# Optimization experiments

Hardware: AMD Instinct MI355X
Metric: run time of the kernel (lower is better)

## Reference

```python
import jax, jax.numpy as jnp
import numpy as np

B, T, H, WD = 512, 168, 512, 4  # batch, seq_len, hidden_dim, WEATHER_DIM


def setup_inputs() -> dict:
    key = jax.random.key(0)
    ks = jax.random.split(key, 11)
    sc = 1.0 / np.sqrt(H)

    def u(k, shape):
        return jax.random.uniform(k, shape, jnp.float32, -sc, sc)

    return {
        "inputs": jax.random.normal(ks[0], (B, T, WD + 1), dtype=jnp.float32),
        # layer 1: input_sz=1 (counts)
        "W1": u(ks[1], (1, 4 * H)),
        "U1": u(ks[2], (H, 4 * H)),
        "V1": u(ks[3], (WD, 4 * H)),
        "b1": u(ks[4], (4 * H,)),
        # layer 2: input_sz=H
        "W2": u(ks[5], (H, 4 * H)),
        "U2": u(ks[6], (H, 4 * H)),
        "V2": u(ks[7], (WD, 4 * H)),
        "b2": u(ks[8], (4 * H,)),
        # final linear head (xavier-ish init)
        "fc_w": u(ks[9], (1, H)),
        "fc_b": jnp.zeros((1,), jnp.float32),
    }


def pew_lstm(x, w, W, U, V, b):
    """Weather-conditioned LSTM layer.
    x: [B,T,I] main input, w: [B,T,WD] weather.
    Gates = x@W + h@U + weather@V + b (weather injected each step).
    Returns hidden sequence [B,T,H]."""
    bs = x.shape[0]
    hdim = U.shape[0]
    # precompute all non-recurrent contributions once: [B,T,4H]
    pre = jnp.einsum('bti,ig->btg', x, W) + jnp.einsum('btw,wg->btg', w, V) + b

    def step(carry, pre_t):
        h, c = carry
        gates = pre_t + h @ U              # [B,4H]
        i, f, g, o = jnp.split(gates, 4, axis=-1)
        c = jax.nn.sigmoid(f) * c + jax.nn.sigmoid(i) * jnp.tanh(g)
        h = jax.nn.sigmoid(o) * jnp.tanh(c)
        return (h, c), h

    h0 = jnp.zeros((bs, hdim), x.dtype)
    (_, _), hs = jax.lax.scan(step, (h0, h0), pre.transpose(1, 0, 2))
    return hs.transpose(1, 0, 2)  # [B,T,H]


def reference(inputs, W1, U1, V1, b1, W2, U2, V2, b2, fc_w, fc_b):
    weather = inputs[:, :, :-1]   # [B,T,WD]
    counts = inputs[:, :, -1:]    # [B,T,1]
    h1 = pew_lstm(counts, weather, W1, U1, V1, b1)
    h2 = pew_lstm(h1, weather, W2, U2, V2, b2)
    out = h2.reshape(-1, h2.shape[-1]) @ fc_w.T + fc_b  # [B*T,1]
    return out.reshape(-1)
```

## Files before the change

kernel.cpp:

```cpp
#include <hip/hip_runtime.h>
#include <cstdint>
#include <cstddef>

typedef unsigned int   u32;
typedef unsigned short u16;
typedef unsigned long long u64;
typedef __attribute__((ext_vector_type(8))) short bf16x8;
typedef __attribute__((ext_vector_type(4))) float f32x4;

#define B_  512
#define T_  168
#define H_  512

#define OFF_U1P   (0u)
#define OFF_UW2P  (2u*1024*1024)
#define OFF_H1    (6u*1024*1024)
#define OFF_H2    (14u*1024*1024)
#define OFF_FLAGS (16u*1024*1024)
#define H_SLOT    262144u
#define NRING     8
#define FSTRIDE   64
#define SMEM_V6   (131072 + 6144 + 3072)

__device__ __forceinline__ u16 f2bf(float v){
  u32 u = __float_as_uint(v);
  return (u16)((u + 0x7fffu + ((u >> 16) & 1u)) >> 16);
}
__device__ __forceinline__ float bf2f(u16 b){ return __uint_as_float(((u32)b) << 16); }
__device__ __forceinline__ float sigm(float x){ return 1.f/(1.f + __expf(-x)); }
__device__ __forceinline__ float tanh_f(float x){
  float e = __expf(-2.f*fabsf(x));
  float t = (1.f - e)/(1.f + e);
  return (x < 0.f) ? -t : t;
}
__device__ __forceinline__ float sigm_f(float x){ return __fdividef(1.f, 1.f + __expf(-x)); }
__device__ __forceinline__ float tanh_ff(float x){
  float e = __expf(-2.f*fabsf(x));
  float t = __fdividef(1.f - e, 1.f + e);
  return (x < 0.f) ? -t : t;
}
__device__ __forceinline__ void spin_ge(int* p, int target){
  while (__hip_atomic_load(p, __ATOMIC_RELAXED, __HIP_MEMORY_SCOPE_AGENT) < target)
    __builtin_amdgcn_s_sleep(1);
}
__device__ __forceinline__ void async_cp16(const void* g, void* l){
  __builtin_amdgcn_global_load_lds((const __attribute__((address_space(1))) u32*)g,
                                   (__attribute__((address_space(3))) u32*)l, 16, 0, 0);
}
__device__ __forceinline__ bf16x8 plain_ld16(const u16* p){
  return *(const bf16x8*)p;
}
__device__ __forceinline__ bf16x8 ring_ld16(const u16* p){
  union { u64 q[2]; bf16x8 v; } u;
  u.q[0] = __hip_atomic_load((const u64*)p,     __ATOMIC_RELAXED, __HIP_MEMORY_SCOPE_AGENT);
  u.q[1] = __hip_atomic_load(((const u64*)p)+1, __ATOMIC_RELAXED, __HIP_MEMORY_SCOPE_AGENT);
  return u.v;
}
__device__ __forceinline__ void ring_st16(u16* p, uint4 v){
  u64 lo = ((u64)v.y << 32) | v.x;
  u64 hi = ((u64)v.w << 32) | v.z;
  __hip_atomic_store((u64*)p,     lo, __ATOMIC_RELAXED, __HIP_MEMORY_SCOPE_AGENT);
  __hip_atomic_store(((u64*)p)+1, hi, __ATOMIC_RELAXED, __HIP_MEMORY_SCOPE_AGENT);
}

__global__ void pack_w_kernel(const float* __restrict__ U1, const float* __restrict__ W2,
                              const float* __restrict__ U2, u16* __restrict__ U1p,
                              u16* __restrict__ UW2p)
{
  int idx = blockIdx.x*256 + threadIdx.x;
  int ln = idx & 63;
  int q8 = ((ln >> 4) << 3);
  int cl = ln & 15;
  if (idx < 16*128*64) {
    int kc = idx >> 13, ng = (idx >> 6) & 127;
    int row0 = kc*32 + q8, col = ng*16 + cl;
    u16* d = U1p + (size_t)idx*8;
    #pragma unroll
    for (int j=0;j<8;j++) d[j] = f2bf(U1[(size_t)(row0+j)*2048 + col]);
  } else {
    int i2 = idx - 16*128*64;
    if (i2 >= 32*128*64) return;
    int kc = i2 >> 13, ng = (i2 >> 6) & 127;
    int row0 = kc*32 + q8, col = ng*16 + cl;
    u16* d = UW2p + (size_t)i2*8;
    #pragma unroll
    for (int j=0;j<8;j++){
      int r = row0 + j;
      float v = (r < 512) ? W2[(size_t)r*2048 + col] : U2[(size_t)(r-512)*2048 + col];
      d[j] = f2bf(v);
    }
  }
}

__global__ void init_kernel(float* __restrict__ out, const float* __restrict__ fcb,
                            int* __restrict__ flags)
{
  int i = blockIdx.x*256 + threadIdx.x;
  if (i < 2048) flags[i] = 0;
  if (i < B_*T_) out[i] = fcb[0];
}


__device__ void run_l1_v6(char* smem, int blk, const float* __restrict__ inp,
                          const float* __restrict__ W1, const float* __restrict__ V,
                          const float* __restrict__ bias, char* __restrict__ ws)
{
  u16*  Bl   = (u16*)smem;
  u16*  hlds = (u16*)(smem + 131072);
  float* wlds = (float*)(smem + 131072 + 6144);
  constexpr int RS = 40;
  const int tid = threadIdx.x, w = tid>>6, ln = tid&63, col = ln&15, quad = ln>>4;
  const int bi = blk & 7, hj = blk >> 3, h0 = hj*32, bg = bi*4 + w;

  const u16* Upak = (const u16*)(ws + OFF_U1P);
  const u16* H1r  = (const u16*)(ws + OFF_H1);
  u16* Hw = (u16*)(ws + OFF_H1);
  int* done1 = (int*)(ws + OFF_FLAGS) + bi*FSTRIDE;
  int* done2 = (int*)(ws + OFF_FLAGS) + 1024 + (bi>>1)*FSTRIDE;

  #pragma unroll
  for (int p=0;p<32;p++){
    int pid = w*32 + p, kc = pid>>3, ngl = pid&7;
    int ng = (ngl>>1)*32 + hj*2 + (ngl&1);
    async_cp16(Upak + ((size_t)(kc*128+ng)*64 + ln)*8, Bl + (size_t)pid*512);
  }
  for (int idx=tid; idx<4*32*6; idx+=256){
    int gate = idx/192, rem = idx%192, hcol = rem/6, k = rem%6;
    int gcol = gate*512 + h0 + hcol;
    wlds[idx] = (k==0)? bias[gcol] : (k<=4 ? V[(size_t)(k-1)*2048 + gcol] : W1[gcol]);
  }

  float c[8];
  #pragma unroll
  for (int i=0;i<8;i++) c[i] = 0.f;
  const f32x4 vzero = {0.f,0.f,0.f,0.f};

  for (int t=0; t<T_; t++){
    if (tid==0){
      if (t>0)      spin_ge(done1, 16*t);
      if (t>=NRING) spin_ge(done2, 32*(t-NRING+1));
      __builtin_amdgcn_fence(__ATOMIC_ACQUIRE, "agent");
    }
    __syncthreads();

    f32x4 acc[8];
    #pragma unroll
    for (int i=0;i<8;i++) acc[i] = vzero;

    if (t > 0){
      const u16* ab = H1r + (size_t)((t-1)&7)*H_SLOT + (size_t)bg*16*512 + (size_t)ln*8;
      bf16x8 aw[8];
      #pragma unroll
      for (int i=0;i<8;i++) aw[i] = plain_ld16(ab + (size_t)i*512);
      #pragma unroll
      for (int kc=0; kc<16; kc++){
        bf16x8 av = aw[kc&7];
        if (kc < 8) aw[kc&7] = plain_ld16(ab + (size_t)(kc+8)*512);
        const u16* bb = Bl + (size_t)kc*8*512 + (size_t)ln*8;
        #pragma unroll
        for (int ngl=0; ngl<8; ngl++)
          acc[ngl] = __builtin_amdgcn_mfma_f32_16x16x32_bf16(
              av, *(const bf16x8*)(bb + (size_t)ngl*512), acc[ngl], 0,0,0);
      }
    }

    float inv[4][5];
    #pragma unroll
    for (int r=0;r<4;r++){
      const float* ip = inp + ((size_t)(bi*64 + w*16 + quad*4 + r)*T_ + t)*5;
      #pragma unroll
      for (int k=0;k<5;k++) inv[r][k] = ip[k];
    }
    #pragma unroll
    for (int hg=0; hg<2; hg++){
      float wv[4][6];
      #pragma unroll
      for (int gate=0; gate<4; gate++){
        const float* wp = wlds + (size_t)(gate*32 + hg*16 + col)*6;
        #pragma unroll
        for (int k=0;k<6;k++) wv[gate][k] = wp[k];
      }
      #pragma unroll
      for (int r=0;r<4;r++){
        float gv[4];
        #pragma unroll
        for (int gate=0; gate<4; gate++){
          gv[gate] = acc[gate*2+hg][r] + wv[gate][0]
                   + inv[r][0]*wv[gate][1] + inv[r][1]*wv[gate][2]
                   + inv[r][2]*wv[gate][3] + inv[r][3]*wv[gate][4]
                   + inv[r][4]*wv[gate][5];
        }
        float ig=sigm_f(gv[0]), fg=sigm_f(gv[1]), gg=tanh_ff(gv[2]), og=sigm_f(gv[3]);
        float cn = fg*c[hg*4+r] + ig*gg;
        c[hg*4+r] = cn;
        hlds[(size_t)(w*16 + quad*4 + r)*RS + hg*16 + col] = f2bf(og*tanh_ff(cn));
      }
    }
    {
      uint4 v = *(const uint4*)&hlds[(size_t)(w*16 + (ln&15))*RS + (ln>>4)*8];
      ring_st16(Hw + (size_t)(t&7)*H_SLOT + ((size_t)(bg*16 + hj)*64 + ln)*8, v);
    }
    __syncthreads();
    if (tid==0){
      __builtin_amdgcn_fence(__ATOMIC_RELEASE, "workgroup");
      __hip_atomic_fetch_add(done1, 1, __ATOMIC_RELAXED, __HIP_MEMORY_SCOPE_AGENT);
    }
  }
}

template<int KCEND>
__device__ __forceinline__ void l2_kloop(f32x4* accA, f32x4* accB, const u16* Bl,
                                         const u16* A1, const u16* A2,
                                         int bgA, int bgB, int ln)
{
  bf16x8 awA[8], awB[8];
  #pragma unroll
  for (int i=0;i<8;i++){
    awA[i] = plain_ld16(A1 + ((size_t)bgA*16 + i)*512 + (size_t)ln*8);
    awB[i] = plain_ld16(A1 + ((size_t)bgB*16 + i)*512 + (size_t)ln*8);
  }
  #pragma unroll
  for (int kc=0; kc<KCEND; kc++){
    bf16x8 avA = awA[kc&7], avB = awB[kc&7];
    if (kc+8 < KCEND){
      int k2 = kc+8;
      const u16* base = (k2 < 16) ? A1 : A2;
      int kcl = (k2 < 16) ? k2 : (k2-16);
      awA[kc&7] = plain_ld16(base + ((size_t)bgA*16 + kcl)*512 + (size_t)ln*8);
      awB[kc&7] = plain_ld16(base + ((size_t)bgB*16 + kcl)*512 + (size_t)ln*8);
    }
    const u16* bb = Bl + (size_t)kc*4*512 + (size_t)ln*8;
    #pragma unroll
    for (int ngl=0; ngl<4; ngl++){
      bf16x8 bf = *(const bf16x8*)(bb + (size_t)ngl*512);
      accA[ngl] = __builtin_amdgcn_mfma_f32_16x16x32_bf16(avA, bf, accA[ngl], 0,0,0);
      accB[ngl] = __builtin_amdgcn_mfma_f32_16x16x32_bf16(avB, bf, accB[ngl], 0,0,0);
    }
  }
}

__device__ void run_l2_v6(char* smem, int blk2, const float* __restrict__ inp,
                          const float* __restrict__ V, const float* __restrict__ bias,
                          const float* __restrict__ fcw, char* __restrict__ ws,
                          float* __restrict__ out)
{
  u16*  Bl   = (u16*)smem;
  u16*  hlds = (u16*)(smem + 131072);
  float* wlds = (float*)(smem + 131072 + 6144);
  constexpr int RS = 24;
  const int tid = threadIdx.x, w = tid>>6, ln = tid&63, col = ln&15, quad = ln>>4;
  const int bi2 = blk2 & 3, hj = blk2 >> 2, h0 = hj*16;
  const int bgA = bi2*8 + w, bgB = bgA + 4;

  const u16* Upak = (const u16*)(ws + OFF_UW2P);
  const u16* H1r  = (const u16*)(ws + OFF_H1);
  const u16* H2r  = (const u16*)(ws + OFF_H2);
  u16* Hw = (u16*)(ws + OFF_H2);
  int* flags = (int*)(ws + OFF_FLAGS);
  int* d1a = flags + (2*bi2)*FSTRIDE;
  int* d1b = flags + (2*bi2+1)*FSTRIDE;
  int* done2 = flags + 1024 + bi2*FSTRIDE;

  #pragma unroll
  for (int p=0;p<32;p++){
    int pid = w*32 + p, kc = pid>>2, ngl = pid&3;
    int ng = ngl*32 + hj;
    async_cp16(Upak + ((size_t)(kc*128+ng)*64 + ln)*8, Bl + (size_t)pid*512);
  }
  for (int idx=tid; idx<4*16*6; idx+=256){
    int gate = idx/96, rem = idx%96, hcol = rem/6, k = rem%6;
    int gcol = gate*512 + h0 + hcol;
    wlds[idx] = (k==0)? bias[gcol] : (k<=4 ? V[(size_t)(k-1)*2048 + gcol] : 0.f);
  }
  const float fcwr = fcw[h0 + col];

  float c[8];
  #pragma unroll
  for (int i=0;i<8;i++) c[i] = 0.f;
  const f32x4 vzero = {0.f,0.f,0.f,0.f};

  for (int t=0; t<T_; t++){
    if (tid==0){
      spin_ge(d1a, 16*(t+1));
      spin_ge(d1b, 16*(t+1));
      if (t>0) spin_ge(done2, 32*t);
      __builtin_amdgcn_fence(__ATOMIC_ACQUIRE, "agent");
    }
    __syncthreads();

    f32x4 accA[4], accB[4];
    #pragma unroll
    for (int i=0;i<4;i++){ accA[i] = vzero; accB[i] = vzero; }

    const u16* A1 = H1r + (size_t)(t&7)*H_SLOT;
    if (t > 0){
      const u16* A2 = H2r + (size_t)((t-1)&1)*H_SLOT;
      l2_kloop<32>(accA, accB, Bl, A1, A2, bgA, bgB, ln);
    } else {
      l2_kloop<16>(accA, accB, Bl, A1, A1, bgA, bgB, ln);
    }

    float wv[4][5];
    #pragma unroll
    for (int gate=0; gate<4; gate++){
      const float* wp = wlds + (size_t)(gate*16 + col)*6;
      #pragma unroll
      for (int k=0;k<5;k++) wv[gate][k] = wp[k];
    }
    float fcp[2][4];
    #pragma unroll
    for (int sel=0; sel<2; sel++){
      const f32x4* ac = sel ? accB : accA;
      #pragma unroll
      for (int r=0;r<4;r++){
        const float* ip = inp + ((size_t)(bi2*128 + sel*64 + w*16 + quad*4 + r)*T_ + t)*5;
        float i0=ip[0], i1=ip[1], i2=ip[2], i3=ip[3];
        float gv[4];
        #pragma unroll
        for (int gate=0; gate<4; gate++){
          gv[gate] = ac[gate][r] + wv[gate][0]
                   + i0*wv[gate][1] + i1*wv[gate][2] + i2*wv[gate][3] + i3*wv[gate][4];
        }
        float ig=sigm_f(gv[0]), fg=sigm_f(gv[1]), gg=tanh_ff(gv[2]), og=sigm_f(gv[3]);
        float cn = fg*c[sel*4+r] + ig*gg;
        c[sel*4+r] = cn;
        float h = og*tanh_ff(cn);
        fcp[sel][r] = h*fcwr;
        hlds[(size_t)(sel*64 + w*16 + quad*4 + r)*RS + col] = f2bf(h);
      }
    }
    #pragma unroll
    for (int sel=0; sel<2; sel++){
      #pragma unroll
      for (int r=0;r<4;r++){
        float v = fcp[sel][r];
        #pragma unroll
        for (int m=1;m<16;m<<=1) v += __shfl_xor(v, m, 16);
        if (col == 0)
          atomicAdd(&out[(size_t)(bi2*128 + sel*64 + w*16 + quad*4 + r)*T_ + t], v);
      }
    }
    {
      int sel = ln>>5, ch = (ln>>4)&1, m = ln&15;
      uint4 v = *(const uint4*)&hlds[(size_t)(sel*64 + w*16 + m)*RS + ch*8];
      int lp = ((hj&1)*2 + ch)*16 + m;
      int bgx = bi2*8 + sel*4 + w;
      ring_st16(Hw + (size_t)(t&1)*H_SLOT + ((size_t)(bgx*16 + (hj>>1))*64 + lp)*8, v);
    }
    __syncthreads();
    if (tid==0){
      __builtin_amdgcn_fence(__ATOMIC_RELEASE, "workgroup");
      __hip_atomic_fetch_add(done2, 1, __ATOMIC_RELAXED, __HIP_MEMORY_SCOPE_AGENT);
    }
  }
}

__global__ void __launch_bounds__(256, 1)
lstm_main_v6(const float* __restrict__ inp, const float* __restrict__ W1,
             const float* __restrict__ V1, const float* __restrict__ b1,
             const float* __restrict__ V2, const float* __restrict__ b2,
             const float* __restrict__ fcw, char* __restrict__ ws, float* __restrict__ out)
{
  extern __shared__ char smem[];
  int blk = blockIdx.x;
  if (blk < 128) run_l1_v6(smem, blk, inp, W1, V1, b1, ws);
  else           run_l2_v6(smem, blk-128, inp, V2, b2, fcw, ws, out);
}

template<int LAYER>
__device__ __forceinline__ void stage_B(u16* buf, const u16* __restrict__ Upak,
                                        int hj, int g, int w, int ln)
{
  constexpr int NGW = (LAYER==1)?16:8;
  constexpr int GKC = (LAYER==1)?2:4;
  #pragma unroll
  for (int p=0;p<8;p++){
    int pid = w*8 + p;
    int kci = pid / NGW;
    int ngl = pid % NGW;
    int gate = ngl / (NGW/4);
    int sub  = ngl % (NGW/4);
    int ng   = gate*32 + hj*(NGW/4) + sub;
    int kc   = g*GKC + kci;
    const u16* src = Upak + ((size_t)(kc*128 + ng)*64 + ln)*8;
    u16* dst = buf + (size_t)(kci*NGW + ngl)*512;
    async_cp16(src, dst);
  }
}

template<int LAYER>
__device__ __forceinline__ void preload_A(bf16x8* areg, const u16* __restrict__ A1,
                                          const u16* __restrict__ A2, int bg, int g, int ln)
{
  constexpr int GKC = (LAYER==1)?2:4;
  #pragma unroll
  for (int kci=0;kci<GKC;kci++){
    int kc = g*GKC + kci;
    const u16* base = A1; int kcl = kc;
    if (LAYER==2 && kc >= 16){ base = A2; kcl = kc - 16; }
    areg[kci] = ring_ld16(base + ((size_t)bg*16 + kcl)*512 + (size_t)ln*8);
  }
}

template<int LAYER>
__device__ void run_layer(u16 (*Bbuf)[16384], int blk,
                          const float* __restrict__ inp,
                          const float* __restrict__ W1,
                          const float* __restrict__ V,
                          const float* __restrict__ bias,
                          const float* __restrict__ fcw,
                          char* __restrict__ ws,
                          float* __restrict__ out)
{
  constexpr int HT  = (LAYER==1)?64:32;
  constexpr int HGN = (LAYER==1)?4:2;
  constexpr int NGW = (LAYER==1)?16:8;
  constexpr int GKC = (LAYER==1)?2:4;
  constexpr int RS  = (LAYER==1)?72:40;
  constexpr int KCP = (LAYER==1)?2:1;
  constexpr int NPIECE = 4*KCP;

  const int tid = threadIdx.x;
  const int w    = tid >> 6;
  const int ln   = tid & 63;
  const int col  = ln & 15;
  const int quad = ln >> 4;
  const int bi = (LAYER==1) ? (blk >> 3) : ((blk-64) >> 4);
  const int hj = (LAYER==1) ? (blk & 7)  : ((blk-64) & 15);
  const int h0 = hj * HT;
  const int bg = bi*4 + w;

  const u16* Upak = (const u16*)(ws + ((LAYER==1)?OFF_U1P:OFF_UW2P));
  const u16* H1r  = (const u16*)(ws + OFF_H1);
  const u16* H2r  = (const u16*)(ws + OFF_H2);
  u16* Hw  = (u16*)(ws + ((LAYER==1)?OFF_H1:OFF_H2));
  int* done1 = (int*)(ws + OFF_FLAGS);
  int* done2 = (int*)(ws + OFF_FLAGS) + 1024;
  u16* hlds  = &Bbuf[0][0];

  float fcwr[HGN];
  if (LAYER==2){
    #pragma unroll
    for (int hg=0; hg<HGN; hg++) fcwr[hg] = fcw[h0 + hg*16 + col];
  }
  float c[HGN*4];
  #pragma unroll
  for (int i=0;i<HGN*4;i++) c[i] = 0.f;
  const f32x4 vzero = {0.f,0.f,0.f,0.f};

  if (LAYER==2) stage_B<LAYER>(Bbuf[0], Upak, hj, 0, w, ln);

  for (int t=0; t<T_; t++){
    if (tid == 0){
      if (LAYER==1){
        if (t > 0)      spin_ge(&done1[bi*FSTRIDE], 8*t);
        if (t >= NRING) spin_ge(&done2[bi*FSTRIDE], 16*(t-NRING+1));
      } else {
        spin_ge(&done1[bi*FSTRIDE], 8*(t+1));
        if (t > 0) spin_ge(&done2[bi*FSTRIDE], 16*t);
      }
      __builtin_amdgcn_fence(__ATOMIC_ACQUIRE, "workgroup");
    }
    __syncthreads();

    f32x4 acc[NGW];
    #pragma unroll
    for (int i=0;i<NGW;i++) acc[i] = vzero;

    const int ngroups = (LAYER==1) ? (t>0 ? 8 : 0) : (t>0 ? 8 : 4);
    if (ngroups > 0){
      const u16* A1; const u16* A2 = nullptr;
      if (LAYER==1) A1 = H1r + (size_t)((t-1)%NRING)*H_SLOT;
      else { A1 = H1r + (size_t)(t%NRING)*H_SLOT;
             if (t>0) A2 = H2r + (size_t)((t-1)&1)*H_SLOT; }

      bf16x8 acur[GKC], anxt[GKC];
      preload_A<LAYER>(acur, A1, A2, bg, 0, ln);
      __syncthreads();
      for (int g=0; g<ngroups; g++){
        if (g+1 < ngroups){
          stage_B<LAYER>(Bbuf[(g+1)&1], Upak, hj, g+1, w, ln);
          preload_A<LAYER>(anxt, A1, A2, bg, g+1, ln);
        }
        #pragma unroll
        for (int kci=0; kci<GKC; kci++){
          const bf16x8 ah = acur[kci];
          #pragma unroll
          for (int ngl=0; ngl<NGW; ngl++){
            const bf16x8 bf = *(const bf16x8*)&Bbuf[g&1][(size_t)(kci*NGW+ngl)*512 + ln*8];
            acc[ngl] = __builtin_amdgcn_mfma_f32_16x16x32_bf16(ah, bf, acc[ngl], 0, 0, 0);
          }
        }
        #pragma unroll
        for (int i=0;i<GKC;i++) acur[i] = anxt[i];
        __syncthreads();
      }
    }

    float inv[4][5];
    #pragma unroll
    for (int r=0;r<4;r++){
      const float* ip = inp + ((size_t)(bi*64 + w*16 + quad*4 + r)*T_ + t)*5;
      #pragma unroll
      for (int k=0;k<5;k++) inv[r][k] = ip[k];
    }
    float fcp[4] = {0.f,0.f,0.f,0.f};
    #pragma unroll
    for (int hg=0; hg<HGN; hg++){
      float wv[4][6];
      #pragma unroll
      for (int gate=0; gate<4; gate++){
        int gcol = gate*512 + h0 + hg*16 + col;
        wv[gate][0] = bias[gcol];
        wv[gate][1] = V[gcol];
        wv[gate][2] = V[2048 + gcol];
        wv[gate][3] = V[4096 + gcol];
        wv[gate][4] = V[6144 + gcol];
        wv[gate][5] = (LAYER==1) ? W1[gcol] : 0.f;
      }
      #pragma unroll
      for (int r=0;r<4;r++){
        float gv[4];
        #pragma unroll
        for (int gate=0; gate<4; gate++){
          float p = wv[gate][0]
                  + inv[r][0]*wv[gate][1] + inv[r][1]*wv[gate][2]
                  + inv[r][2]*wv[gate][3] + inv[r][3]*wv[gate][4];
          if (LAYER==1) p += inv[r][4]*wv[gate][5];
          gv[gate] = acc[gate*HGN + hg][r] + p;
        }
        float ig = sigm(gv[0]);
        float fg = sigm(gv[1]);
        float gg = tanh_f(gv[2]);
        float og = sigm(gv[3]);
        float cn = fg*c[hg*4+r] + ig*gg;
        c[hg*4+r] = cn;
        float h = og*tanh_f(cn);
        if (LAYER==2) fcp[r] += h*fcwr[hg];
        int bl = w*16 + quad*4 + r;
        int hc = hg*16 + col;
        hlds[bl*RS + hc] = f2bf(h);
      }
    }
    if (LAYER==2){
      #pragma unroll
      for (int r=0;r<4;r++){
        #pragma unroll
        for (int m=1;m<16;m<<=1) fcp[r] += __shfl_xor(fcp[r], m, 16);
      }
      if (col == 0){
        #pragma unroll
        for (int r=0;r<4;r++)
          atomicAdd(&out[(size_t)(bi*64 + w*16 + quad*4 + r)*T_ + t], fcp[r]);
      }
    }
    __syncthreads();

    {
      u16* dst = Hw + (size_t)((LAYER==1) ? (t % NRING) : (t & 1))*H_SLOT;
      #pragma unroll
      for (int it=0; it<(NPIECE*64+255)/256; it++){
        int cidx = tid + it*256;
        if (cidx < NPIECE*64){
          int piece = cidx >> 6, lp = cidx & 63;
          int bgi, kci;
          if (LAYER==1){ bgi = (piece >> 1) & 3; kci = piece & 1; }
          else         { bgi = piece & 3;        kci = 0; }
          int row = bgi*16 + (lp & 15);
          int hc  = kci*32 + ((lp >> 4) << 3);
          uint4 v = *(const uint4*)&hlds[(size_t)row*RS + hc];
          int kcg = (LAYER==1) ? (hj*2 + kci) : hj;
          ring_st16(&dst[(((size_t)(bi*4 + bgi)*16 + kcg)*64 + lp)*8], v);
        }
      }
    }
    __syncthreads();
    if (tid == 0){
      __builtin_amdgcn_fence(__ATOMIC_RELEASE, "workgroup");
      int* dp = (LAYER==1) ? &done1[bi*FSTRIDE] : &done2[bi*FSTRIDE];
      __hip_atomic_fetch_add(dp, 1, __ATOMIC_RELAXED, __HIP_MEMORY_SCOPE_AGENT);
    }
    if (t+1 < T_) stage_B<LAYER>(Bbuf[0], Upak, hj, 0, w, ln);
  }
}

__global__ void __launch_bounds__(256, 1)
lstm_main_v5(const float* __restrict__ inp, const float* __restrict__ W1,
             const float* __restrict__ V1, const float* __restrict__ b1,
             const float* __restrict__ V2, const float* __restrict__ b2,
             const float* __restrict__ fcw, char* __restrict__ ws, float* __restrict__ out)
{
  __shared__ __align__(16) u16 Bbuf[2][16384];
  int blk = blockIdx.x;
  if (blk < 64) run_layer<1>(Bbuf, blk, inp, W1, V1, b1, nullptr, ws, out);
  else          run_layer<2>(Bbuf, blk, inp, nullptr, V2, b2, fcw, ws, out);
}

extern "C" void kernel_launch(void* const* d_in, const int* in_sizes, int n_in,
                              void* d_out, int out_size, void* d_ws, size_t ws_size,
                              hipStream_t stream) {
  const float* inp = (const float*)d_in[0];
  const float* W1  = (const float*)d_in[1];
  const float* U1  = (const float*)d_in[2];
  const float* V1  = (const float*)d_in[3];
  const float* b1  = (const float*)d_in[4];
  const float* W2  = (const float*)d_in[5];
  const float* U2  = (const float*)d_in[6];
  const float* V2  = (const float*)d_in[7];
  const float* b2  = (const float*)d_in[8];
  const float* fcw = (const float*)d_in[9];
  const float* fcb = (const float*)d_in[10];
  char* ws = (char*)d_ws;
  float* out = (float*)d_out;

  pack_w_kernel<<<1536, 256, 0, stream>>>(U1, W2, U2,
      (u16*)(ws + OFF_U1P), (u16*)(ws + OFF_UW2P));
  init_kernel<<<(B_*T_ + 255)/256, 256, 0, stream>>>(out, fcb, (int*)(ws + OFF_FLAGS));

  int dev = 0; (void)hipGetDevice(&dev);
  int maxShm = 0;
  (void)hipDeviceGetAttribute(&maxShm, hipDeviceAttributeMaxSharedMemoryPerBlock, dev);
  if (maxShm >= SMEM_V6) {
    (void)hipFuncSetAttribute((const void*)lstm_main_v6,
                              hipFuncAttributeMaxDynamicSharedMemorySize, SMEM_V6);
    lstm_main_v6<<<256, 256, SMEM_V6, stream>>>(inp, W1, V1, b1, V2, b2, fcw, ws, out);
  } else {
    lstm_main_v5<<<192, 256, 0, stream>>>(inp, W1, V1, b1, V2, b2, fcw, ws, out);
  }
}
```

Baseline: 2.254 ms.

## Replace block-wide counter sync with per-wave flags and XCD-aware block placement

Result: slower. 3.237 ms (+43.6%).

```diff
diff --git a/kernel.cpp b/kernel.cpp
--- a/kernel.cpp
+++ b/kernel.cpp
@@ -14,24 +14,19 @@
 
 #define OFF_U1P   (0u)
 #define OFF_UW2P  (2u*1024*1024)
-#define OFF_H1    (6u*1024*1024)
-#define OFF_H2    (14u*1024*1024)
-#define OFF_FLAGS (16u*1024*1024)
+#define OFF_FLAGS (6u*1024*1024)
+#define OFF_TICK  (6u*1024*1024 + 256u*1024)
+#define OFF_H1    (8u*1024*1024)
+#define OFF_H2    (12u*1024*1024)
 #define H_SLOT    262144u
 #define NRING     8
-#define FSTRIDE   64
-#define SMEM_V6   (131072 + 6144 + 3072)
+#define FS        32
+#define NFLAG     16384
+#define SMEM_V8   (131072 + 6144 + 3072)
 
 __device__ __forceinline__ u16 f2bf(float v){
   u32 u = __float_as_uint(v);
   return (u16)((u + 0x7fffu + ((u >> 16) & 1u)) >> 16);
-}
-__device__ __forceinline__ float bf2f(u16 b){ return __uint_as_float(((u32)b) << 16); }
-__device__ __forceinline__ float sigm(float x){ return 1.f/(1.f + __expf(-x)); }
-__device__ __forceinline__ float tanh_f(float x){
-  float e = __expf(-2.f*fabsf(x));
-  float t = (1.f - e)/(1.f + e);
-  return (x < 0.f) ? -t : t;
 }
 __device__ __forceinline__ float sigm_f(float x){ return __fdividef(1.f, 1.f + __expf(-x)); }
 __device__ __forceinline__ float tanh_ff(float x){
@@ -39,28 +34,63 @@
   float t = __fdividef(1.f - e, 1.f + e);
   return (x < 0.f) ? -t : t;
 }
-__device__ __forceinline__ void spin_ge(int* p, int target){
-  while (__hip_atomic_load(p, __ATOMIC_RELAXED, __HIP_MEMORY_SCOPE_AGENT) < target)
-    __builtin_amdgcn_s_sleep(1);
-}
 __device__ __forceinline__ void async_cp16(const void* g, void* l){
   __builtin_amdgcn_global_load_lds((const __attribute__((address_space(1))) u32*)g,
                                    (__attribute__((address_space(3))) u32*)l, 16, 0, 0);
 }
-__device__ __forceinline__ bf16x8 plain_ld16(const u16* p){
-  return *(const bf16x8*)p;
-}
-__device__ __forceinline__ bf16x8 ring_ld16(const u16* p){
+
+
+__device__ __forceinline__ int ld_sc0(const int* p){
+  int v;
+  asm volatile("global_load_dword %0, %1, off sc0\n\ts_waitcnt vmcnt(0)"
+               : "=v"(v) : "v"(p) : "memory");
+  return v;
+}
+__device__ __forceinline__ void inv_l1c(){
+  asm volatile("buffer_inv sc0" ::: "memory");
+}
+__device__ __forceinline__ void cfence(){
+  __builtin_amdgcn_fence(__ATOMIC_ACQUIRE, "workgroup");
+}
+__device__ __forceinline__ void drain_vm(){
+  asm volatile("s_waitcnt vmcnt(0)" ::: "memory");
+}
+__device__ __forceinline__ void poll_ge(const int* p, bool act, int target,
+                                        bool local, int& vlast){
+  if (__all((!act) || (vlast >= target))) return;
+  int it = 0;
+  while (true){
+    int v = 0x7fffffff;
+    if (act){
+      if (local && ((it & 7) != 7)) v = ld_sc0(p);
+      else v = __hip_atomic_load(p, __ATOMIC_RELAXED, __HIP_MEMORY_SCOPE_AGENT);
+    }
+    if (__all(v >= target)){ vlast = v; break; }
+    it++;
+    __builtin_amdgcn_s_sleep(1);
+  }
+}
+template<bool LOCAL>
+__device__ __forceinline__ bf16x8 ldh(const u16* p){
+  if (LOCAL) return *(const bf16x8*)p;
   union { u64 q[2]; bf16x8 v; } u;
   u.q[0] = __hip_atomic_load((const u64*)p,     __ATOMIC_RELAXED, __HIP_MEMORY_SCOPE_AGENT);
   u.q[1] = __hip_atomic_load(((const u64*)p)+1, __ATOMIC_RELAXED, __HIP_MEMORY_SCOPE_AGENT);
   return u.v;
 }
-__device__ __forceinline__ void ring_st16(u16* p, uint4 v){
+__device__ __forceinline__ void st16_dual(u16* p, uint4 v, bool dual){
   u64 lo = ((u64)v.y << 32) | v.x;
   u64 hi = ((u64)v.w << 32) | v.z;
-  __hip_atomic_store((u64*)p,     lo, __ATOMIC_RELAXED, __HIP_MEMORY_SCOPE_AGENT);
-  __hip_atomic_store(((u64*)p)+1, hi, __ATOMIC_RELAXED, __HIP_MEMORY_SCOPE_AGENT);
+  ((volatile u64*)p)[0] = lo;
+  ((volatile u64*)p)[1] = hi;
+  if (dual){
+    __hip_atomic_store((u64*)p,     lo, __ATOMIC_RELAXED, __HIP_MEMORY_SCOPE_AGENT);
+    __hip_atomic_store(((u64*)p)+1, hi, __ATOMIC_RELAXED, __HIP_MEMORY_SCOPE_AGENT);
+  }
+}
+__device__ __forceinline__ void post_flag(int* p, int v){
+  *(volatile int*)p = v;
+  __hip_atomic_store(p, v, __ATOMIC_RELAXED, __HIP_MEMORY_SCOPE_AGENT);
 }
 
 __global__ void pack_w_kernel(const float* __restrict__ U1, const float* __restrict__ W2,
@@ -93,30 +123,31 @@
 }
 
 __global__ void init_kernel(float* __restrict__ out, const float* __restrict__ fcb,
-                            int* __restrict__ flags)
+                            int* __restrict__ flags, int* __restrict__ tick)
 {
   int i = blockIdx.x*256 + threadIdx.x;
-  if (i < 2048) flags[i] = 0;
+  if (i < 2*NFLAG) flags[i] = 0;
+  if (i < 16) tick[i] = 0;
   if (i < B_*T_) out[i] = fcb[0];
 }
 
-
-__device__ void run_l1_v6(char* smem, int blk, const float* __restrict__ inp,
-                          const float* __restrict__ W1, const float* __restrict__ V,
-                          const float* __restrict__ bias, char* __restrict__ ws)
+template<bool LOCAL>
+__device__ void run_l1(char* smem, int bi, int hj, const float* __restrict__ inp,
+                       const float* __restrict__ W1, const float* __restrict__ V,
+                       const float* __restrict__ bias, char* __restrict__ ws)
 {
   u16*  Bl   = (u16*)smem;
   u16*  hlds = (u16*)(smem + 131072);
   float* wlds = (float*)(smem + 131072 + 6144);
   constexpr int RS = 40;
   const int tid = threadIdx.x, w = tid>>6, ln = tid&63, col = ln&15, quad = ln>>4;
-  const int bi = blk & 7, hj = blk >> 3, h0 = hj*32, bg = bi*4 + w;
+  const int h0 = hj*32, bg = bi*4 + w;
 
   const u16* Upak = (const u16*)(ws + OFF_U1P);
   const u16* H1r  = (const u16*)(ws + OFF_H1);
   u16* Hw = (u16*)(ws + OFF_H1);
-  int* done1 = (int*)(ws + OFF_FLAGS) + bi*FSTRIDE;
-  int* done2 = (int*)(ws + OFF_FLAGS) + 1024 + (bi>>1)*FSTRIDE;
+  int* flag1 = (int*)(ws + OFF_FLAGS);
+  int* flag2 = flag1 + NFLAG;
 
   #pragma unroll
   for (int p=0;p<32;p++){
@@ -130,32 +161,35 @@
     wlds[idx] = (k==0)? bias[gcol] : (k<=4 ? V[(size_t)(k-1)*2048 + gcol] : W1[gcol]);
   }
 
+  const int* f1p = flag1 + (size_t)((bi*16 + (ln&15))*4 + w)*FS;
+  const int* f2p = flag2 + (size_t)(((bi>>1)*32 + (ln&31))*4 + w)*FS;
+  int* myf = flag1 + (size_t)((bi*16 + hj)*4 + w)*FS;
+  const bool a16 = ln < 16, a32 = ln < 32;
+  int vl_f1 = 0, vl_bp = 0;
+
   float c[8];
   #pragma unroll
   for (int i=0;i<8;i++) c[i] = 0.f;
   const f32x4 vzero = {0.f,0.f,0.f,0.f};
 
+  __syncthreads();
+
   for (int t=0; t<T_; t++){
-    if (tid==0){
-      if (t>0)      spin_ge(done1, 16*t);
-      if (t>=NRING) spin_ge(done2, 32*(t-NRING+1));
-      __builtin_amdgcn_fence(__ATOMIC_ACQUIRE, "agent");
-    }
-    __syncthreads();
-
     f32x4 acc[8];
     #pragma unroll
     for (int i=0;i<8;i++) acc[i] = vzero;
 
     if (t > 0){
+      poll_ge(f1p, a16, t, LOCAL, vl_f1);
+      if (LOCAL) inv_l1c(); else cfence();
       const u16* ab = H1r + (size_t)((t-1)&7)*H_SLOT + (size_t)bg*16*512 + (size_t)ln*8;
       bf16x8 aw[8];
       #pragma unroll
-      for (int i=0;i<8;i++) aw[i] = plain_ld16(ab + (size_t)i*512);
+      for (int i=0;i<8;i++) aw[i] = ldh<LOCAL>(ab + (size_t)i*512);
       #pragma unroll
       for (int kc=0; kc<16; kc++){
         bf16x8 av = aw[kc&7];
-        if (kc < 8) aw[kc&7] = plain_ld16(ab + (size_t)(kc+8)*512);
+        if (kc < 8) aw[kc&7] = ldh<LOCAL>(ab + (size_t)(kc+8)*512);
         const u16* bb = Bl + (size_t)kc*8*512 + (size_t)ln*8;
         #pragma unroll
         for (int ngl=0; ngl<8; ngl++)
@@ -164,12 +198,12 @@
       }
     }
 
-    float inv[4][5];
+    float iv[4][5];
     #pragma unroll
     for (int r=0;r<4;r++){
       const float* ip = inp + ((size_t)(bi*64 + w*16 + quad*4 + r)*T_ + t)*5;
       #pragma unroll
-      for (int k=0;k<5;k++) inv[r][k] = ip[k];
+      for (int k=0;k<5;k++) iv[r][k] = ip[k];
     }
     #pragma unroll
     for (int hg=0; hg<2; hg++){
@@ -186,9 +220,9 @@
         #pragma unroll
         for (int gate=0; gate<4; gate++){
           gv[gate] = acc[gate*2+hg][r] + wv[gate][0]
-                   + inv[r][0]*wv[gate][1] + inv[r][1]*wv[gate][2]
-                   + inv[r][2]*wv[gate][3] + inv[r][3]*wv[gate][4]
-                   + inv[r][4]*wv[gate][5];
+                   + iv[r][0]*wv[gate][1] + iv[r][1]*wv[gate][2]
+                   + iv[r][2]*wv[gate][3] + iv[r][3]*wv[gate][4]
+                   + iv[r][4]*wv[gate][5];
         }
         float ig=sigm_f(gv[0]), fg=sigm_f(gv[1]), gg=tanh_ff(gv[2]), og=sigm_f(gv[3]);
         float cn = fg*c[hg*4+r] + ig*gg;
@@ -196,40 +230,37 @@
         hlds[(size_t)(w*16 + quad*4 + r)*RS + hg*16 + col] = f2bf(og*tanh_ff(cn));
       }
     }
+    if (t >= NRING) poll_ge(f2p, a32, t-NRING+1, false, vl_bp);
     {
       uint4 v = *(const uint4*)&hlds[(size_t)(w*16 + (ln&15))*RS + (ln>>4)*8];
-      ring_st16(Hw + (size_t)(t&7)*H_SLOT + ((size_t)(bg*16 + hj)*64 + ln)*8, v);
-    }
-    __syncthreads();
-    if (tid==0){
-      __builtin_amdgcn_fence(__ATOMIC_RELEASE, "workgroup");
-      __hip_atomic_fetch_add(done1, 1, __ATOMIC_RELAXED, __HIP_MEMORY_SCOPE_AGENT);
-    }
-  }
-}
-
-template<int KCEND>
-__device__ __forceinline__ void l2_kloop(f32x4* accA, f32x4* accB, const u16* Bl,
-                                         const u16* A1, const u16* A2,
-                                         int bgA, int bgB, int ln)
-{
+      u16* dst = Hw + (size_t)(t&7)*H_SLOT + ((size_t)(bg*16 + hj)*64 + ln)*8;
+      st16_dual(dst, v, true);
+    }
+    drain_vm();
+    if (ln == 0) post_flag(myf, t+1);
+  }
+}
+
+template<bool LOC>
+__device__ __forceinline__ void l2_half(f32x4* accA, f32x4* accB, const u16* Bh,
+                                        const u16* A, int bgA, int bgB, int ln)
+{
+  const u16* pA = A + (size_t)bgA*16*512 + (size_t)ln*8;
+  const u16* pB = A + (size_t)bgB*16*512 + (size_t)ln*8;
   bf16x8 awA[8], awB[8];
   #pragma unroll
   for (int i=0;i<8;i++){
-    awA[i] = plain_ld16(A1 + ((size_t)bgA*16 + i)*512 + (size_t)ln*8);
-    awB[i] = plain_ld16(A1 + ((size_t)bgB*16 + i)*512 + (size_t)ln*8);
-  }
-  #pragma unroll
-  for (int kc=0; kc<KCEND; kc++){
+    awA[i] = ldh<LOC>(pA + (size_t)i*512);
+    awB[i] = ldh<LOC>(pB + (size_t)i*512);
+  }
+  #pragma unroll
+  for (int kc=0; kc<16; kc++){
     bf16x8 avA = awA[kc&7], avB = awB[kc&7];
-    if (kc+8 < KCEND){
-      int k2 = kc+8;
-      const u16* base = (k2 < 16) ? A1 : A2;
-      int kcl = (k2 < 16) ? k2 : (k2-16);
-      awA[kc&7] = plain_ld16(base + ((size_t)bgA*16 + kcl)*512 + (size_t)ln*8);
-      awB[kc&7] = plain_ld16(base + ((size_t)bgB*16 + kcl)*512 + (size_t)ln*8);
-    }
-    const u16* bb = Bl + (size_t)kc*4*512 + (size_t)ln*8;
+    if (kc < 8){
+      awA[kc&7] = ldh<LOC>(pA + (size_t)(kc+8)*512);
+      awB[kc&7] = ldh<LOC>(pB + (size_t)(kc+8)*512);
+    }
+    const u16* bb = Bh + (size_t)kc*4*512 + (size_t)ln*8;
     #pragma unroll
     for (int ngl=0; ngl<4; ngl++){
       bf16x8 bf = *(const bf16x8*)(bb + (size_t)ngl*512);
@@ -239,27 +270,25 @@
   }
 }
 
-__device__ void run_l2_v6(char* smem, int blk2, const float* __restrict__ inp,
-                          const float* __restrict__ V, const float* __restrict__ bias,
-                          const float* __restrict__ fcw, char* __restrict__ ws,
-                          float* __restrict__ out)
+template<bool LOCAL>
+__device__ void run_l2(char* smem, int bi2, int hj, const float* __restrict__ inp,
+                       const float* __restrict__ V, const float* __restrict__ bias,
+                       const float* __restrict__ fcw, char* __restrict__ ws,
+                       float* __restrict__ out)
 {
   u16*  Bl   = (u16*)smem;
   u16*  hlds = (u16*)(smem + 131072);
   float* wlds = (float*)(smem + 131072 + 6144);
   constexpr int RS = 24;
   const int tid = threadIdx.x, w = tid>>6, ln = tid&63, col = ln&15, quad = ln>>4;
-  const int bi2 = blk2 & 3, hj = blk2 >> 2, h0 = hj*16;
-  const int bgA = bi2*8 + w, bgB = bgA + 4;
+  const int h0 = hj*16, bgA = bi2*8 + w, bgB = bgA + 4;
 
   const u16* Upak = (const u16*)(ws + OFF_UW2P);
   const u16* H1r  = (const u16*)(ws + OFF_H1);
   const u16* H2r  = (const u16*)(ws + OFF_H2);
   u16* Hw = (u16*)(ws + OFF_H2);
-  int* flags = (int*)(ws + OFF_FLAGS);
-  int* d1a = flags + (2*bi2)*FSTRIDE;
-  int* d1b = flags + (2*bi2+1)*FSTRIDE;
-  int* done2 = flags + 1024 + bi2*FSTRIDE;
+  int* flag1 = (int*)(ws + OFF_FLAGS);
+  int* flag2 = flag1 + NFLAG;
 
   #pragma unroll
   for (int p=0;p<32;p++){
@@ -274,30 +303,34 @@
   }
   const float fcwr = fcw[h0 + col];
 
+  const int* h1f = flag1 + (size_t)(((2*bi2 + ((ln>>4)&1))*16 + (ln&15))*4 + w)*FS;
+  const int* h2f = flag2 + (size_t)((bi2*32 + (ln&31))*4 + w)*FS;
+  int* myf = flag2 + (size_t)((bi2*32 + hj)*4 + w)*FS;
+  const bool a32 = ln < 32;
+  int vl_h1 = 0, vl_h2 = 0;
+
   float c[8];
   #pragma unroll
   for (int i=0;i<8;i++) c[i] = 0.f;
   const f32x4 vzero = {0.f,0.f,0.f,0.f};
 
+  __syncthreads();
+
   for (int t=0; t<T_; t++){
-    if (tid==0){
-      spin_ge(d1a, 16*(t+1));
-      spin_ge(d1b, 16*(t+1));
-      if (t>0) spin_ge(done2, 32*t);
-      __builtin_amdgcn_fence(__ATOMIC_ACQUIRE, "agent");
-    }
-    __syncthreads();
-
     f32x4 accA[4], accB[4];
     #pragma unroll
     for (int i=0;i<4;i++){ accA[i] = vzero; accB[i] = vzero; }
 
+    poll_ge(h1f, a32, t+1, false, vl_h1);
+    cfence();
     const u16* A1 = H1r + (size_t)(t&7)*H_SLOT;
+    l2_half<false>(accA, accB, Bl, A1, bgA, bgB, ln);
+
     if (t > 0){
-      const u16* A2 = H2r + (size_t)((t-1)&1)*H_SLOT;
-      l2_kloop<32>(accA, accB, Bl, A1, A2, bgA, bgB, ln);
-    } else {
-      l2_kloop<16>(accA, accB, Bl, A1, A1, bgA, bgB, ln);
+      poll_ge(h2f, a32, t, LOCAL, vl_h2);
+      if (LOCAL) inv_l1c(); else cfence();
+      const u16* A2 = H2r + (size_t)((t-1)&7)*H_SLOT;
+      l2_half<LOCAL>(accA, accB, Bl + (size_t)16*4*512, A2, bgA, bgB, ln);
     }
 
     float wv[4][5];
@@ -329,6 +362,17 @@
         hlds[(size_t)(sel*64 + w*16 + quad*4 + r)*RS + col] = f2bf(h);
       }
     }
+    {
+      int sel = ln>>5, ch = (ln>>4)&1, m = ln&15;
+      uint4 v = *(const uint4*)&hlds[(size_t)(sel*64 + w*16 + m)*RS + ch*8];
+      int lp = ((hj&1)*2 + ch)*16 + m;
+      int bgx = bi2*8 + sel*4 + w;
+      u16* dst = Hw + (size_t)(t&7)*H_SLOT + ((size_t)(bgx*16 + (hj>>1))*64 + lp)*8;
+      st16_dual(dst, v, !LOCAL);
+    }
+    drain_vm();
+    if (ln == 0) post_flag(myf, t+1);
+
     #pragma unroll
     for (int sel=0; sel<2; sel++){
       #pragma unroll
@@ -340,265 +384,59 @@
           atomicAdd(&out[(size_t)(bi2*128 + sel*64 + w*16 + quad*4 + r)*T_ + t], v);
       }
     }
-    {
-      int sel = ln>>5, ch = (ln>>4)&1, m = ln&15;
-      uint4 v = *(const uint4*)&hlds[(size_t)(sel*64 + w*16 + m)*RS + ch*8];
-      int lp = ((hj&1)*2 + ch)*16 + m;
-      int bgx = bi2*8 + sel*4 + w;
-      ring_st16(Hw + (size_t)(t&1)*H_SLOT + ((size_t)(bgx*16 + (hj>>1))*64 + lp)*8, v);
-    }
-    __syncthreads();
-    if (tid==0){
-      __builtin_amdgcn_fence(__ATOMIC_RELEASE, "workgroup");
-      __hip_atomic_fetch_add(done2, 1, __ATOMIC_RELAXED, __HIP_MEMORY_SCOPE_AGENT);
-    }
   }
 }
 
 __global__ void __launch_bounds__(256, 1)
-lstm_main_v6(const float* __restrict__ inp, const float* __restrict__ W1,
+lstm_main_v8(const float* __restrict__ inp, const float* __restrict__ W1,
              const float* __restrict__ V1, const float* __restrict__ b1,
              const float* __restrict__ V2, const float* __restrict__ b2,
              const float* __restrict__ fcw, char* __restrict__ ws, float* __restrict__ out)
 {
   extern __shared__ char smem[];
-  int blk = blockIdx.x;
-  if (blk < 128) run_l1_v6(smem, blk, inp, W1, V1, b1, ws);
-  else           run_l2_v6(smem, blk-128, inp, V2, b2, fcw, ws, out);
-}
-
-template<int LAYER>
-__device__ __forceinline__ void stage_B(u16* buf, const u16* __restrict__ Upak,
-                                        int hj, int g, int w, int ln)
-{
-  constexpr int NGW = (LAYER==1)?16:8;
-  constexpr int GKC = (LAYER==1)?2:4;
-  #pragma unroll
-  for (int p=0;p<8;p++){
-    int pid = w*8 + p;
-    int kci = pid / NGW;
-    int ngl = pid % NGW;
-    int gate = ngl / (NGW/4);
-    int sub  = ngl % (NGW/4);
-    int ng   = gate*32 + hj*(NGW/4) + sub;
-    int kc   = g*GKC + kci;
-    const u16* src = Upak + ((size_t)(kc*128 + ng)*64 + ln)*8;
-    u16* dst = buf + (size_t)(kci*NGW + ngl)*512;
-    async_cp16(src, dst);
-  }
-}
-
-template<int LAYER>
-__device__ __forceinline__ void preload_A(bf16x8* areg, const u16* __restrict__ A1,
-                                          const u16* __restrict__ A2, int bg, int g, int ln)
-{
-  constexpr int GKC = (LAYER==1)?2:4;
-  #pragma unroll
-  for (int kci=0;kci<GKC;kci++){
-    int kc = g*GKC + kci;
-    const u16* base = A1; int kcl = kc;
-    if (LAYER==2 && kc >= 16){ base = A2; kcl = kc - 16; }
-    areg[kci] = ring_ld16(base + ((size_t)bg*16 + kcl)*512 + (size_t)ln*8);
-  }
-}
-
-template<int LAYER>
-__device__ void run_layer(u16 (*Bbuf)[16384], int blk,
-                          const float* __restrict__ inp,
-                          const float* __restrict__ W1,
-                          const float* __restrict__ V,
-                          const float* __restrict__ bias,
-                          const float* __restrict__ fcw,
-                          char* __restrict__ ws,
-                          float* __restrict__ out)
-{
-  constexpr int HT  = (LAYER==1)?64:32;
-  constexpr int HGN = (LAYER==1)?4:2;
-  constexpr int NGW = (LAYER==1)?16:8;
-  constexpr int GKC = (LAYER==1)?2:4;
-  constexpr int RS  = (LAYER==1)?72:40;
-  constexpr int KCP = (LAYER==1)?2:1;
-  constexpr int NPIECE = 4*KCP;
-
-  const int tid = threadIdx.x;
-  const int w    = tid >> 6;
-  const int ln   = tid & 63;
-  const int col  = ln & 15;
-  const int quad = ln >> 4;
-  const int bi = (LAYER==1) ? (blk >> 3) : ((blk-64) >> 4);
-  const int hj = (LAYER==1) ? (blk & 7)  : ((blk-64) & 15);
-  const int h0 = hj * HT;
-  const int bg = bi*4 + w;
-
-  const u16* Upak = (const u16*)(ws + ((LAYER==1)?OFF_U1P:OFF_UW2P));
-  const u16* H1r  = (const u16*)(ws + OFF_H1);
-  const u16* H2r  = (const u16*)(ws + OFF_H2);
-  u16* Hw  = (u16*)(ws + ((LAYER==1)?OFF_H1:OFF_H2));
-  int* done1 = (int*)(ws + OFF_FLAGS);
-  int* done2 = (int*)(ws + OFF_FLAGS) + 1024;
-  u16* hlds  = &Bbuf[0][0];
-
-  float fcwr[HGN];
-  if (LAYER==2){
-    #pragma unroll
-    for (int hg=0; hg<HGN; hg++) fcwr[hg] = fcw[h0 + hg*16 + col];
-  }
-  float c[HGN*4];
-  #pragma unroll
-  for (int i=0;i<HGN*4;i++) c[i] = 0.f;
-  const f32x4 vzero = {0.f,0.f,0.f,0.f};
-
-  if (LAYER==2) stage_B<LAYER>(Bbuf[0], Upak, hj, 0, w, ln);
-
-  for (int t=0; t<T_; t++){
-    if (tid == 0){
-      if (LAYER==1){
-        if (t > 0)      spin_ge(&done1[bi*FSTRIDE], 8*t);
-        if (t >= NRING) spin_ge(&done2[bi*FSTRIDE], 16*(t-NRING+1));
-      } else {
-        spin_ge(&done1[bi*FSTRIDE], 8*(t+1));
-        if (t > 0) spin_ge(&done2[bi*FSTRIDE], 16*t);
-      }
-      __builtin_amdgcn_fence(__ATOMIC_ACQUIRE, "workgroup");
-    }
-    __syncthreads();
-
-    f32x4 acc[NGW];
-    #pragma unroll
-    for (int i=0;i<NGW;i++) acc[i] = vzero;
-
-    const int ngroups = (LAYER==1) ? (t>0 ? 8 : 0) : (t>0 ? 8 : 4);
-    if (ngroups > 0){
-      const u16* A1; const u16* A2 = nullptr;
-      if (LAYER==1) A1 = H1r + (size_t)((t-1)%NRING)*H_SLOT;
-      else { A1 = H1r + (size_t)(t%NRING)*H_SLOT;
-             if (t>0) A2 = H2r + (size_t)((t-1)&1)*H_SLOT; }
-
-      bf16x8 acur[GKC], anxt[GKC];
-      preload_A<LAYER>(acur, A1, A2, bg, 0, ln);
-      __syncthreads();
-      for (int g=0; g<ngroups; g++){
-        if (g+1 < ngroups){
-          stage_B<LAYER>(Bbuf[(g+1)&1], Upak, hj, g+1, w, ln);
-          preload_A<LAYER>(anxt, A1, A2, bg, g+1, ln);
-        }
-        #pragma unroll
-        for (int kci=0; kci<GKC; kci++){
-          const bf16x8 ah = acur[kci];
-          #pragma unroll
-          for (int ngl=0; ngl<NGW; ngl++){
-            const bf16x8 bf = *(const bf16x8*)&Bbuf[g&1][(size_t)(kci*NGW+ngl)*512 + ln*8];
-            acc[ngl] = __builtin_amdgcn_mfma_f32_16x16x32_bf16(ah, bf, acc[ngl], 0, 0, 0);
-          }
-        }
-        #pragma unroll
-        for (int i=0;i<GKC;i++) acur[i] = anxt[i];
-        __syncthreads();
-      }
-    }
-
-    float inv[4][5];
-    #pragma unroll
-    for (int r=0;r<4;r++){
-      const float* ip = inp + ((size_t)(bi*64 + w*16 + quad*4 + r)*T_ + t)*5;
-      #pragma unroll
-      for (int k=0;k<5;k++) inv[r][k] = ip[k];
-    }
-    float fcp[4] = {0.f,0.f,0.f,0.f};
-    #pragma unroll
-    for (int hg=0; hg<HGN; hg++){
-      float wv[4][6];
-      #pragma unroll
-      for (int gate=0; gate<4; gate++){
-        int gcol = gate*512 + h0 + hg*16 + col;
-        wv[gate][0] = bias[gcol];
-        wv[gate][1] = V[gcol];
-        wv[gate][2] = V[2048 + gcol];
-        wv[gate][3] = V[4096 + gcol];
-        wv[gate][4] = V[6144 + gcol];
-        wv[gate][5] = (LAYER==1) ? W1[gcol] : 0.f;
-      }
-      #pragma unroll
-      for (int r=0;r<4;r++){
-        float gv[4];
-        #pragma unroll
-        for (int gate=0; gate<4; gate++){
-          float p = wv[gate][0]
-                  + inv[r][0]*wv[gate][1] + inv[r][1]*wv[gate][2]
-                  + inv[r][2]*wv[gate][3] + inv[r][3]*wv[gate][4];
-          if (LAYER==1) p += inv[r][4]*wv[gate][5];
-          gv[gate] = acc[gate*HGN + hg][r] + p;
-        }
-        float ig = sigm(gv[0]);
-        float fg = sigm(gv[1]);
-        float gg = tanh_f(gv[2]);
-        float og = sigm(gv[3]);
-        float cn = fg*c[hg*4+r] + ig*gg;
-        c[hg*4+r] = cn;
-        float h = og*tanh_f(cn);
-        if (LAYER==2) fcp[r] += h*fcwr[hg];
-        int bl = w*16 + quad*4 + r;
-        int hc = hg*16 + col;
-        hlds[bl*RS + hc] = f2bf(h);
-      }
-    }
-    if (LAYER==2){
-      #pragma unroll
-      for (int r=0;r<4;r++){
-        #pragma unroll
-        for (int m=1;m<16;m<<=1) fcp[r] += __shfl_xor(fcp[r], m, 16);
-      }
-      if (col == 0){
-        #pragma unroll
-        for (int r=0;r<4;r++)
-          atomicAdd(&out[(size_t)(bi*64 + w*16 + quad*4 + r)*T_ + t], fcp[r]);
-      }
-    }
-    __syncthreads();
-
-    {
-      u16* dst = Hw + (size_t)((LAYER==1) ? (t % NRING) : (t & 1))*H_SLOT;
-      #pragma unroll
-      for (int it=0; it<(NPIECE*64+255)/256; it++){
-        int cidx = tid + it*256;
-        if (cidx < NPIECE*64){
-          int piece = cidx >> 6, lp = cidx & 63;
-          int bgi, kci;
-          if (LAYER==1){ bgi = (piece >> 1) & 3; kci = piece & 1; }
-          else         { bgi = piece & 3;        kci = 0; }
-          int row = bgi*16 + (lp & 15);
-          int hc  = kci*32 + ((lp >> 4) << 3);
-          uint4 v = *(const uint4*)&hlds[(size_t)row*RS + hc];
-          int kcg = (LAYER==1) ? (hj*2 + kci) : hj;
-          ring_st16(&dst[(((size_t)(bi*4 + bgi)*16 + kcg)*64 + lp)*8], v);
-        }
-      }
-    }
-    __syncthreads();
-    if (tid == 0){
-      __builtin_amdgcn_fence(__ATOMIC_RELEASE, "workgroup");
-      int* dp = (LAYER==1) ? &done1[bi*FSTRIDE] : &done2[bi*FSTRIDE];
-      __hip_atomic_fetch_add(dp, 1, __ATOMIC_RELAXED, __HIP_MEMORY_SCOPE_AGENT);
-    }
-    if (t+1 < T_) stage_B<LAYER>(Bbuf[0], Upak, hj, 0, w, ln);
-  }
-}
-
-__global__ void __launch_bounds__(256, 1)
-lstm_main_v5(const float* __restrict__ inp, const float* __restrict__ W1,
-             const float* __restrict__ V1, const float* __restrict__ b1,
-             const float* __restrict__ V2, const float* __restrict__ b2,
-             const float* __restrict__ fcw, char* __restrict__ ws, float* __restrict__ out)
-{
-  __shared__ __align__(16) u16 Bbuf[2][16384];
-  int blk = blockIdx.x;
-  if (blk < 64) run_layer<1>(Bbuf, blk, inp, W1, V1, b1, nullptr, ws, out);
-  else          run_layer<2>(Bbuf, blk, inp, nullptr, V2, b2, fcw, ws, out);
+  __shared__ int sh_pos, sh_loc;
+  if (threadIdx.x == 0){
+    int xcd;
+    asm volatile("s_getreg_b32 %0, hwreg(HW_REG_XCC_ID)" : "=s"(xcd));
+    xcd &= 7;
+    int* tick = (int*)(ws + OFF_TICK);
+    int rank = __hip_atomic_fetch_add(&tick[xcd], 1, __ATOMIC_RELAXED, __HIP_MEMORY_SCOPE_AGENT);
+    __hip_atomic_fetch_add(&tick[8], 1, __ATOMIC_RELAXED, __HIP_MEMORY_SCOPE_AGENT);
+    while (__hip_atomic_load(&tick[8], __ATOMIC_RELAXED, __HIP_MEMORY_SCOPE_AGENT) < 256)
+      __builtin_amdgcn_s_sleep(8);
+    int cc[8], pref = 0;
+    #pragma unroll
+    for (int x=0;x<8;x++)
+      cc[x] = __hip_atomic_load(&tick[x], __ATOMIC_RELAXED, __HIP_MEMORY_SCOPE_AGENT);
+    for (int x=0;x<xcd;x++) pref += cc[x];
+    int pos = pref + rank;
+    int lo, hi;
+    if (pos < 128){ lo = (pos>>4)<<4; hi = lo + 16; }
+    else { int q = pos - 128; lo = 128 + ((q>>5)<<5); hi = lo + 32; }
+    int xlo = 7, xhi = 7, s = 0;
+    for (int x=0;x<8;x++){ int e = s + cc[x];
+      if (lo   >= s && lo   < e) xlo = x;
+      if (hi-1 >= s && hi-1 < e) xhi = x;
+      s = e; }
+    sh_loc = (xlo == xcd && xhi == xcd) ? 1 : 0;
+    sh_pos = pos;
+  }
+  __syncthreads();
+  const int pos = sh_pos, loc = sh_loc;
+  if (pos < 128){
+    if (loc) run_l1<true >(smem, pos>>4, pos&15, inp, W1, V1, b1, ws);
+    else     run_l1<false>(smem, pos>>4, pos&15, inp, W1, V1, b1, ws);
+  } else {
+    int q = pos - 128;
+    if (loc) run_l2<true >(smem, q>>5, q&31, inp, V2, b2, fcw, ws, out);
+    else     run_l2<false>(smem, q>>5, q&31, inp, V2, b2, fcw, ws, out);
+  }
 }
 
 extern "C" void kernel_launch(void* const* d_in, const int* in_sizes, int n_in,
                               void* d_out, int out_size, void* d_ws, size_t ws_size,
                               hipStream_t stream) {
+  (void)in_sizes; (void)n_in; (void)out_size; (void)ws_size;
   const float* inp = (const float*)d_in[0];
   const float* W1  = (const float*)d_in[1];
   const float* U1  = (const float*)d_in[2];
@@ -615,16 +453,9 @@
 
   pack_w_kernel<<<1536, 256, 0, stream>>>(U1, W2, U2,
       (u16*)(ws + OFF_U1P), (u16*)(ws + OFF_UW2P));
-  init_kernel<<<(B_*T_ + 255)/256, 256, 0, stream>>>(out, fcb, (int*)(ws + OFF_FLAGS));
-
-  int dev = 0; (void)hipGetDevice(&dev);
-  int maxShm = 0;
-  (void)hipDeviceGetAttribute(&maxShm, hipDeviceAttributeMaxSharedMemoryPerBlock, dev);
-  if (maxShm >= SMEM_V6) {
-    (void)hipFuncSetAttribute((const void*)lstm_main_v6,
-                              hipFuncAttributeMaxDynamicSharedMemorySize, SMEM_V6);
-    lstm_main_v6<<<256, 256, SMEM_V6, stream>>>(inp, W1, V1, b1, V2, b2, fcw, ws, out);
-  } else {
-    lstm_main_v5<<<192, 256, 0, stream>>>(inp, W1, V1, b1, V2, b2, fcw, ws, out);
-  }
-}
+  init_kernel<<<(B_*T_ + 255)/256, 256, 0, stream>>>(out, fcb,
+      (int*)(ws + OFF_FLAGS), (int*)(ws + OFF_TICK));
+  (void)hipFuncSetAttribute((const void*)lstm_main_v8,
+                            hipFuncAttributeMaxDynamicSharedMemorySize, SMEM_V8);
+  lstm_main_v8<<<256, 256, SMEM_V8, stream>>>(inp, W1, V1, b1, V2, b2, fcw, ws, out);
+}
```
